# Kernel tuning notes

Hardware: AMD Instinct MI355X
Metric: run time of the kernel (lower is better)

## Reference

```python
import jax, jax.numpy as jnp
import numpy as np

DIM = 64   # flow dimension
HID = 8    # hidden_dim=[8]
B = 131072 # batch of samples


def setup_inputs() -> dict:
    key = jax.random.key(0)
    ks = jax.random.split(key, 6)
    L = DIM - 1  # number of per-dim MLPs (layers[0..L-1], layer l has fan-in l+1)
    lim = float(np.sqrt(0.5))
    x = jax.random.normal(ks[0], (B, DIM), jnp.float32)
    initial_param = jax.random.uniform(ks[1], (2,), jnp.float32, -lim, lim)
    # Ragged Linear(fan_in=l+1, 8) weights stacked into padded [L, HID, L];
    # entries beyond column l are masked to zero in reference().
    fan_in = np.arange(1, DIM).astype(np.float32)          # (L,)
    bnd1 = (1.0 / np.sqrt(fan_in))[:, None, None]          # torch Linear default init bound
    W1 = jax.random.uniform(ks[2], (L, HID, L), jnp.float32, -1.0, 1.0) * bnd1
    b1 = jax.random.uniform(ks[3], (L, HID), jnp.float32, -1.0, 1.0) * bnd1[:, :, 0]
    bnd2 = 1.0 / np.sqrt(HID)
    W2 = jax.random.uniform(ks[4], (L, 2, HID), jnp.float32, -bnd2, bnd2)
    b2 = jax.random.uniform(ks[5], (L, 2), jnp.float32, -bnd2, bnd2)
    return {"x": x, "initial_param": initial_param, "W1": W1, "b1": b1, "W2": W2, "b2": b2}


def reference(x, initial_param, W1, b1, W2, b2):
    B_, D = x.shape
    L = W1.shape[0]  # D - 1
    # mask[l, d] = 1 iff d <= l  ->  layer l sees exactly x[:, :l+1]
    mask = jnp.tril(jnp.ones((L, L), x.dtype))
    W1m = W1 * mask[:, None, :]
    # all dim-1 tiny MLPs fused into two batched contractions
    h = jnp.tanh(jnp.einsum('bd,lhd->blh', x[:, :L], W1m) + b1)   # [B, L, HID]
    out = jnp.einsum('blh,loh->blo', h, W2) + b2                   # [B, L, 2]
    mu0 = jnp.broadcast_to(initial_param[0], (B_, 1)).astype(x.dtype)
    al0 = jnp.broadcast_to(initial_param[1], (B_, 1)).astype(x.dtype)
    mu = jnp.concatenate([mu0, out[:, :, 0]], axis=1)              # [B, D]
    alpha = jnp.concatenate([al0, out[:, :, 1]], axis=1)           # [B, D]
    z = x * jnp.exp(alpha) + mu
    log_det = jnp.sum(alpha, axis=1)
    return z, log_det
```

## Files before the change

### kernel.cpp

```cpp
#include <hip/hip_runtime.h>


#define DIMS 64

typedef __attribute__((ext_vector_type(8))) short short8;
typedef __attribute__((ext_vector_type(4))) float f32x4;
typedef __attribute__((ext_vector_type(4))) unsigned int uint4v;
typedef unsigned short ushort_t;
typedef unsigned int uint_t;

#if __has_builtin(__builtin_amdgcn_exp2f)
#define YSCALE 2.8853900817779268f
#define EXPY(x) __builtin_amdgcn_exp2f(x)
#else
#define YSCALE 2.0f
#define EXPY(x) __expf(x)
#endif

__device__ __forceinline__ uint_t pk2bf(float a, float b) {
#if __has_builtin(__builtin_amdgcn_cvt_pk_bf16_f32)
    typedef __attribute__((ext_vector_type(2))) __bf16 bf16x2;
    bf16x2 r = __builtin_amdgcn_cvt_pk_bf16_f32(a, b);
    return __builtin_bit_cast(uint_t, r);
#else
    uint_t ua = __float_as_uint(a); ua += 0x7FFFu + ((ua >> 16) & 1u);
    uint_t ub = __float_as_uint(b); ub += 0x7FFFu + ((ub >> 16) & 1u);
    return (ub & 0xFFFF0000u) | (ua >> 16);
#endif
}

__device__ __forceinline__ ushort_t f2bf(float f) {
    uint_t u = __float_as_uint(f);
    u += 0x7FFFu + ((u >> 16) & 1u);
    return (ushort_t)(u >> 16);
}

#define W2F_OFF (512 * 64)
#define FREG_OFF (512 * 64 + 128 * 64)
#define PREP_N (512 * 64 + 128 * 64 + 512 + 128)

__device__ __forceinline__ int logrow(int p) {
    int n = p & 15;
    return (p >> 5) * 32 + (n >> 2) * 8 + ((p >> 4) & 1) * 4 + (n & 3);
}

__global__ void siaf_prep(const float* __restrict__ W1, const float* __restrict__ b1,
                          const float* __restrict__ W2, const float* __restrict__ b2,
                          ushort_t* __restrict__ ws_u) {
    ushort_t* w1b    = ws_u;
    ushort_t* w2full = ws_u + W2F_OFF;
    float*    fb     = (float*)(ws_u + FREG_OFF);
    int i = blockIdx.x * 256 + threadIdx.x;
    if (i < 512 * 64) {
        int k = i & 63, p = i >> 6;
        int L = logrow(p), l = L >> 3, h = L & 7;
        float v = 0.0f;
        if (l < 63 && k <= l) v = W1[(l * 8 + h) * 63 + k] * YSCALE;
        w1b[i] = f2bf(v);
    } else if (i < FREG_OFF) {
        int j = i - W2F_OFF;
        int kl = j & 63, r = j >> 6, l = r >> 1, o = r & 1;
        float v = 0.0f;
        if (l < 63 && (kl >> 3) == (l & 7)) v = W2[(l * 2 + o) * 8 + (kl & 7)];
        w2full[j] = f2bf(v);
    } else if (i < FREG_OFF + 512) {
        int p = i - FREG_OFF;
        int L = logrow(p), l = L >> 3, h = L & 7;
        fb[p] = (l < 63) ? b1[l * 8 + h] * YSCALE : 0.0f;
    } else if (i < PREP_N) {
        int j = i - (FREG_OFF + 512);
        int l = j >> 1, o = j & 1;
        fb[512 + j] = (l < 63) ? b2[l * 2 + o] : 0.0f;
    }
}

__device__ __forceinline__ float th(float t) {
    float e = EXPY(t);
    float r = __builtin_amdgcn_rcpf(e + 1.0f);
    return fmaf(-2.0f, r, 1.0f);
}

__global__ __launch_bounds__(256, 5) void siaf_mfma(
        const float* __restrict__ x, const float* __restrict__ ip,
        const ushort_t* __restrict__ ws_u, float* __restrict__ out, int nB) {
    const ushort_t* w1b    = ws_u;
    const ushort_t* w2full = ws_u + W2F_OFF;
    const float*    b1f    = (const float*)(ws_u + FREG_OFF);
    const float*    b2f    = b1f + 512;

    __shared__ float xz[4][32 * 64];

    const int tid  = threadIdx.x;
    const int wv   = tid >> 6, lane = tid & 63;
    const int s16  = lane & 15, quad = lane >> 4;
    const int sbase = blockIdx.x * 128 + wv * 32;

    float* xzw = xz[wv];

    #pragma unroll
    for (int g = 0; g < 8; ++g) {
        const float4 v = ((const float4*)(x + (size_t)(sbase + 4 * g) * DIMS))[lane];
        const int s_loc = 4 * g + quad;
        const int chunk = (lane & 15) ^ (s_loc & 15);
        *(float4*)(xzw + s_loc * 64 + chunk * 4) = v;
    }

    const float ip0 = ip[0], ip1 = ip[1];

    short8 bfr[2][2];
    float lsum[2] = {0.0f, 0.0f};
    #pragma unroll
    for (int st = 0; st < 2; ++st) {
        const int s_loc = st * 16 + s16;
        #pragma unroll
        for (int kh = 0; kh < 2; ++kh) {
            const int c0 = kh * 8 + quad * 2;
            float4 va = *(const float4*)(xzw + s_loc * 64 + ((c0 ^ s16) & 15) * 4);
            float4 vb = *(const float4*)(xzw + s_loc * 64 + (((c0 + 1) ^ s16) & 15) * 4);
            uint4v u = {pk2bf(va.x, va.y), pk2bf(va.z, va.w),
                        pk2bf(vb.x, vb.y), pk2bf(vb.z, vb.w)};
            bfr[st][kh] = __builtin_bit_cast(short8, u);
        }
    }

    for (int mt = 0; mt < 8; ++mt) {
        const ushort_t* w2p = w2full + (mt * 16 + s16) * 64 + quad * 8;
        f32x4 acc2[2] = {{0.f, 0.f, 0.f, 0.f}, {0.f, 0.f, 0.f, 0.f}};

        #pragma unroll
        for (int half = 0; half < 2; ++half) {
            const int p0 = mt * 4 + half * 2;
            const ushort_t* w1p0 = w1b + (p0 * 16 + s16) * 64 + quad * 8;
            const ushort_t* w1p1 = w1p0 + 1024;
            const short8 a00 = *(const short8*)w1p0;
            const short8 a10 = *(const short8*)w1p1;
            const float4 bi0 = *(const float4*)(b1f + p0 * 16 + quad * 4);
            const float4 bi1 = *(const float4*)(b1f + (p0 + 1) * 16 + quad * 4);
            const short8 c2 = *(const short8*)(w2p + half * 32);
            short8 a01, a11;
            if (mt >= 4) {
                a01 = *(const short8*)(w1p0 + 32);
                a11 = *(const short8*)(w1p1 + 32);
            }
            #pragma unroll
            for (int st = 0; st < 2; ++st) {
                f32x4 aE = {bi0.x, bi0.y, bi0.z, bi0.w};
                f32x4 aO = {bi1.x, bi1.y, bi1.z, bi1.w};
                aE = __builtin_amdgcn_mfma_f32_16x16x32_bf16(a00, bfr[st][0], aE, 0, 0, 0);
                aO = __builtin_amdgcn_mfma_f32_16x16x32_bf16(a10, bfr[st][0], aO, 0, 0, 0);
                if (mt >= 4) {
                    aE = __builtin_amdgcn_mfma_f32_16x16x32_bf16(a01, bfr[st][1], aE, 0, 0, 0);
                    aO = __builtin_amdgcn_mfma_f32_16x16x32_bf16(a11, bfr[st][1], aO, 0, 0, 0);
                }
                uint4v hh = {pk2bf(th(aE[0]), th(aE[1])), pk2bf(th(aE[2]), th(aE[3])),
                             pk2bf(th(aO[0]), th(aO[1])), pk2bf(th(aO[2]), th(aO[3]))};
                const short8 hfr = __builtin_bit_cast(short8, hh);
                acc2[st] = __builtin_amdgcn_mfma_f32_16x16x32_bf16(c2, hfr, acc2[st], 0, 0, 0);
            }
        }

        const int l0 = mt * 8 + quad * 2;
        const float4 b2v = *(const float4*)(b2f + l0 * 2);
        const bool pad = (l0 == 62);
        #pragma unroll
        for (int st = 0; st < 2; ++st) {
            const int s_loc = st * 16 + s16;
            float mu0 = acc2[st][0] + b2v.x, al0 = acc2[st][1] + b2v.y;
            float mu1 = acc2[st][2] + b2v.z, al1 = acc2[st][3] + b2v.w;
            const int d1 = l0 + 1;
            float* p1 = xzw + s_loc * 64 + (((((d1 >> 2) ^ s16) & 15) << 2) | (d1 & 3));
            *p1 = fmaf(*p1, __expf(al0), mu0);
            lsum[st] += al0;
            const float alB = pad ? ip1 : al1;
            const float muB = pad ? ip0 : mu1;
            const int d2 = pad ? 0 : (l0 + 2);
            float* p2 = xzw + s_loc * 64 + (((((d2 >> 2) ^ s16) & 15) << 2) | (d2 & 3));
            *p2 = fmaf(*p2, __expf(alB), muB);
            lsum[st] += alB;
        }
    }

    #pragma unroll
    for (int g = 0; g < 8; ++g) {
        const int s_loc = 4 * g + quad;
        const int chunk = (lane & 15) ^ (s_loc & 15);
        const float4 v = *(const float4*)(xzw + s_loc * 64 + chunk * 4);
        ((float4*)(out + (size_t)(sbase + 4 * g) * DIMS))[lane] = v;
    }

    #pragma unroll
    for (int st = 0; st < 2; ++st) {
        float v = lsum[st];
        int r1 = __builtin_amdgcn_ds_swizzle(__float_as_int(v), 0x401F);
        v += __int_as_float(r1);
        int r2 = __builtin_amdgcn_ds_bpermute((lane ^ 32) << 2, __float_as_int(v));
        v += __int_as_float(r2);
        if (quad == 0)
            out[(size_t)nB * DIMS + sbase + st * 16 + s16] = v;
    }
}

extern "C" void kernel_launch(void* const* d_in, const int* in_sizes, int n_in,
                              void* d_out, int out_size, void* d_ws, size_t ws_size,
                              hipStream_t stream) {
    const float* x  = (const float*)d_in[0];
    const float* ip = (const float*)d_in[1];
    const float* W1 = (const float*)d_in[2];
    const float* b1 = (const float*)d_in[3];
    const float* W2 = (const float*)d_in[4];
    const float* b2 = (const float*)d_in[5];
    ushort_t* ws = (ushort_t*)d_ws;
    float* out = (float*)d_out;

    const int nB = in_sizes[0] / DIMS;

    siaf_prep<<<(PREP_N + 255) / 256, 256, 0, stream>>>(W1, b1, W2, b2, ws);
    siaf_mfma<<<nB / 128, 256, 0, stream>>>(x, ip, ws, out, nB);
}
```

Baseline: 130.0 us.

## Stage compacted swizzled weights in LDS and use 512-thread blocks

Weights are repacked into a compact, XOR-swizzled layout with the zero half dropped for the first eight groups. Each block copies this layout into LDS once and reads MFMA fragments from shared memory instead of global/L2. Blocks grow to 512 threads covering 256 samples, and the mt loop is fully unrolled. The cost is about 68KB of extra LDS per block, which lowers occupancy, plus a prologue copy and sync before any work starts.

```diff
diff --git a/kernel.cpp b/kernel.cpp
--- a/kernel.cpp
+++ b/kernel.cpp
@@ -2,6 +2,7 @@
 
 
 #define DIMS 64
+#define TPB  512
 
 typedef __attribute__((ext_vector_type(8))) short short8;
 typedef __attribute__((ext_vector_type(4))) float f32x4;
@@ -16,6 +17,17 @@
 #define YSCALE 2.0f
 #define EXPY(x) __expf(x)
 #endif
+
+#define A_OFF 0
+#define B_OFF 16384
+#define C_OFF 49152
+#define D_OFF 65536
+#define E_OFF 67584
+#define WT_BYTES 68096
+#define WT_CHUNKS (WT_BYTES / 16)
+#define XZ_OFF WT_BYTES
+#define LDS_BYTES (WT_BYTES + 8 * 32 * DIMS * 4)
+#define PREP_N (32768 + 640)
 
 __device__ __forceinline__ uint_t pk2bf(float a, float b) {
 #if __has_builtin(__builtin_amdgcn_cvt_pk_bf16_f32)
@@ -35,10 +47,6 @@
     return (ushort_t)(u >> 16);
 }
 
-#define W2F_OFF (512 * 64)
-#define FREG_OFF (512 * 64 + 128 * 64)
-#define PREP_N (512 * 64 + 128 * 64 + 512 + 128)
-
 __device__ __forceinline__ int logrow(int p) {
     int n = p & 15;
     return (p >> 5) * 32 + (n >> 2) * 8 + ((p >> 4) & 1) * 4 + (n & 3);
@@ -47,30 +55,43 @@
 __global__ void siaf_prep(const float* __restrict__ W1, const float* __restrict__ b1,
                           const float* __restrict__ W2, const float* __restrict__ b2,
                           ushort_t* __restrict__ ws_u) {
-    ushort_t* w1b    = ws_u;
-    ushort_t* w2full = ws_u + W2F_OFF;
-    float*    fb     = (float*)(ws_u + FREG_OFF);
     int i = blockIdx.x * 256 + threadIdx.x;
-    if (i < 512 * 64) {
-        int k = i & 63, p = i >> 6;
+    if (i < 8192) {
+        int p = i >> 5, e = i & 31;
+        int cp = e >> 3, j = e & 7;
+        int k = ((cp ^ (p & 3)) << 3) | j;
         int L = logrow(p), l = L >> 3, h = L & 7;
-        float v = 0.0f;
-        if (l < 63 && k <= l) v = W1[(l * 8 + h) * 63 + k] * YSCALE;
-        w1b[i] = f2bf(v);
-    } else if (i < FREG_OFF) {
-        int j = i - W2F_OFF;
-        int kl = j & 63, r = j >> 6, l = r >> 1, o = r & 1;
+        float v = (k <= l) ? W1[(l * 8 + h) * 63 + k] * YSCALE : 0.0f;
+        ws_u[i] = f2bf(v);
+    } else if (i < 24576) {
+        int v_ = i - 8192;
+        int p = 256 + (v_ >> 6), e = v_ & 63;
+        int cp = e >> 3, j = e & 7;
+        int k = ((cp ^ (p & 7)) << 3) | j;
+        int L = logrow(p), l = L >> 3, h = L & 7;
+        float v = (l < 63 && k <= l) ? W1[(l * 8 + h) * 63 + k] * YSCALE : 0.0f;
+        ws_u[i] = f2bf(v);
+    } else if (i < 32768) {
+        int j_ = i - 24576;
+        int r = j_ >> 6, e = j_ & 63;
+        int cp = e >> 3, jj = e & 7;
+        int kl = ((cp ^ (r & 7)) << 3) | jj;
+        int l = r >> 1, o = r & 1;
         float v = 0.0f;
         if (l < 63 && (kl >> 3) == (l & 7)) v = W2[(l * 2 + o) * 8 + (kl & 7)];
-        w2full[j] = f2bf(v);
-    } else if (i < FREG_OFF + 512) {
-        int p = i - FREG_OFF;
-        int L = logrow(p), l = L >> 3, h = L & 7;
-        fb[p] = (l < 63) ? b1[l * 8 + h] * YSCALE : 0.0f;
+        ws_u[i] = f2bf(v);
     } else if (i < PREP_N) {
-        int j = i - (FREG_OFF + 512);
-        int l = j >> 1, o = j & 1;
-        fb[512 + j] = (l < 63) ? b2[l * 2 + o] : 0.0f;
+        int f = i - 32768;
+        float* fws = (float*)(ws_u + 32768);
+        float v = 0.0f;
+        if (f < 512) {
+            int L = logrow(f), l = L >> 3, h = L & 7;
+            if (l < 63) v = b1[l * 8 + h] * YSCALE;
+        } else {
+            int j = f - 512, l = j >> 1, o = j & 1;
+            if (l < 63) v = b2[l * 2 + o];
+        }
+        fws[f] = v;
     }
 }
 
@@ -80,31 +101,36 @@
     return fmaf(-2.0f, r, 1.0f);
 }
 
-__global__ __launch_bounds__(256, 5) void siaf_mfma(
+__global__ __launch_bounds__(TPB, 2) void siaf_main(
         const float* __restrict__ x, const float* __restrict__ ip,
-        const ushort_t* __restrict__ ws_u, float* __restrict__ out, int nB) {
-    const ushort_t* w1b    = ws_u;
-    const ushort_t* w2full = ws_u + W2F_OFF;
-    const float*    b1f    = (const float*)(ws_u + FREG_OFF);
-    const float*    b2f    = b1f + 512;
-
-    __shared__ float xz[4][32 * 64];
+        const uint4* __restrict__ wsv, float* __restrict__ out, int nB) {
+    extern __shared__ unsigned char lds[];
+
+    {
+        uint4* dst = (uint4*)lds;
+        for (int c = threadIdx.x; c < WT_CHUNKS; c += TPB) dst[c] = wsv[c];
+    }
+    __syncthreads();
+
+    const ushort_t* wA  = (const ushort_t*)(lds + A_OFF);
+    const ushort_t* wB  = (const ushort_t*)(lds + B_OFF);
+    const ushort_t* wC  = (const ushort_t*)(lds + C_OFF);
+    const float*    b1f = (const float*)(lds + D_OFF);
+    const float*    b2f = (const float*)(lds + E_OFF);
 
     const int tid  = threadIdx.x;
     const int wv   = tid >> 6, lane = tid & 63;
     const int s16  = lane & 15, quad = lane >> 4;
-    const int sbase = blockIdx.x * 128 + wv * 32;
-
-    float* xzw = xz[wv];
+    const int sbase = blockIdx.x * 256 + wv * 32;
+    float* xzw = (float*)(lds + XZ_OFF) + wv * (32 * DIMS);
 
     #pragma unroll
     for (int g = 0; g < 8; ++g) {
         const float4 v = ((const float4*)(x + (size_t)(sbase + 4 * g) * DIMS))[lane];
         const int s_loc = 4 * g + quad;
-        const int chunk = (lane & 15) ^ (s_loc & 15);
+        const int chunk = s16 ^ (s_loc & 15);
         *(float4*)(xzw + s_loc * 64 + chunk * 4) = v;
     }
-
     const float ip0 = ip[0], ip1 = ip[1];
 
     short8 bfr[2][2];
@@ -123,32 +149,40 @@
         }
     }
 
+    #pragma unroll
     for (int mt = 0; mt < 8; ++mt) {
-        const ushort_t* w2p = w2full + (mt * 16 + s16) * 64 + quad * 8;
         f32x4 acc2[2] = {{0.f, 0.f, 0.f, 0.f}, {0.f, 0.f, 0.f, 0.f}};
 
         #pragma unroll
         for (int half = 0; half < 2; ++half) {
-            const int p0 = mt * 4 + half * 2;
-            const ushort_t* w1p0 = w1b + (p0 * 16 + s16) * 64 + quad * 8;
-            const ushort_t* w1p1 = w1p0 + 1024;
-            const short8 a00 = *(const short8*)w1p0;
-            const short8 a10 = *(const short8*)w1p1;
+            const int g = 2 * mt + half;
+            const int p0 = 2 * g;
+            short8 a00, a10, a01{}, a11{};
+            if (g < 8) {
+                const ushort_t* rowp = wA + (g * 32 + s16) * 32;
+                const int pc = quad ^ (s16 & 3);
+                a00 = *(const short8*)(rowp + pc * 8);
+                a10 = *(const short8*)(rowp + 512 + pc * 8);
+            } else {
+                const ushort_t* rowp = wB + ((g - 8) * 32 + s16) * 64;
+                const int pc = quad ^ (s16 & 7);
+                a00 = *(const short8*)(rowp + pc * 8);
+                a10 = *(const short8*)(rowp + 1024 + pc * 8);
+                a01 = *(const short8*)(rowp + (pc ^ 4) * 8);
+                a11 = *(const short8*)(rowp + 1024 + (pc ^ 4) * 8);
+            }
             const float4 bi0 = *(const float4*)(b1f + p0 * 16 + quad * 4);
             const float4 bi1 = *(const float4*)(b1f + (p0 + 1) * 16 + quad * 4);
-            const short8 c2 = *(const short8*)(w2p + half * 32);
-            short8 a01, a11;
-            if (mt >= 4) {
-                a01 = *(const short8*)(w1p0 + 32);
-                a11 = *(const short8*)(w1p1 + 32);
-            }
+            const short8 c2 = *(const short8*)(
+                wC + (mt * 16 + s16) * 64 + ((half * 4 + quad) ^ (s16 & 7)) * 8);
+
             #pragma unroll
             for (int st = 0; st < 2; ++st) {
                 f32x4 aE = {bi0.x, bi0.y, bi0.z, bi0.w};
                 f32x4 aO = {bi1.x, bi1.y, bi1.z, bi1.w};
                 aE = __builtin_amdgcn_mfma_f32_16x16x32_bf16(a00, bfr[st][0], aE, 0, 0, 0);
                 aO = __builtin_amdgcn_mfma_f32_16x16x32_bf16(a10, bfr[st][0], aO, 0, 0, 0);
-                if (mt >= 4) {
+                if (g >= 8) {
                     aE = __builtin_amdgcn_mfma_f32_16x16x32_bf16(a01, bfr[st][1], aE, 0, 0, 0);
                     aO = __builtin_amdgcn_mfma_f32_16x16x32_bf16(a11, bfr[st][1], aO, 0, 0, 0);
                 }
@@ -183,7 +217,7 @@
     #pragma unroll
     for (int g = 0; g < 8; ++g) {
         const int s_loc = 4 * g + quad;
-        const int chunk = (lane & 15) ^ (s_loc & 15);
+        const int chunk = s16 ^ (s_loc & 15);
         const float4 v = *(const float4*)(xzw + s_loc * 64 + chunk * 4);
         ((float4*)(out + (size_t)(sbase + 4 * g) * DIMS))[lane] = v;
     }
@@ -211,9 +245,13 @@
     const float* b2 = (const float*)d_in[5];
     ushort_t* ws = (ushort_t*)d_ws;
     float* out = (float*)d_out;
+    (void)ws_size;
 
     const int nB = in_sizes[0] / DIMS;
 
+    (void)hipFuncSetAttribute((const void*)siaf_main,
+                              hipFuncAttributeMaxDynamicSharedMemorySize, LDS_BYTES);
+
     siaf_prep<<<(PREP_N + 255) / 256, 256, 0, stream>>>(W1, b1, W2, b2, ws);
-    siaf_mfma<<<nB / 128, 256, 0, stream>>>(x, ip, ws, out, nB);
-}
+    siaf_main<<<nB / 256, TPB, LDS_BYTES, stream>>>(x, ip, (const uint4*)ws, out, nB);
+}
```

After: 121.4 us. -6.7%, faster.
